# Kernel tuning notes

Hardware: AMD Instinct MI355X
Metric: run time of the kernel (lower is better)

Reference implementation:

```python
import jax, jax.numpy as jnp
import numpy as np

N_NODES = 100000
N_EDGES = 640000
H = 128

def setup_inputs() -> dict:
    key = jax.random.key(0)
    k = jax.random.split(key, 8)
    x_src = jax.random.normal(k[0], (N_NODES, H), dtype=jnp.float32)
    x_dst = jax.random.normal(k[1], (N_NODES, H), dtype=jnp.float32)
    src_idx = jax.random.randint(k[2], (N_EDGES,), 0, N_NODES, dtype=jnp.int64)
    dst_idx = jax.random.randint(k[3], (N_EDGES,), 0, N_NODES, dtype=jnp.int64)
    # torch Linear default init: U(-1/sqrt(fan_in), 1/sqrt(fan_in)); randn*scale is fine for a numeric baseline
    W1 = jax.random.normal(k[4], (H, 2 * H), dtype=jnp.float32) * (1.0 / np.sqrt(2 * H))
    b1 = jnp.zeros((H,), dtype=jnp.float32)
    W2 = jax.random.normal(k[5], (1, H), dtype=jnp.float32) * (1.0 / np.sqrt(H))
    b2 = jnp.zeros((1,), dtype=jnp.float32)
    return {"x_src": x_src, "x_dst": x_dst, "src_idx": src_idx, "dst_idx": dst_idx,
            "W1": W1, "b1": b1, "W2": W2, "b2": b2}

def reference(x_src, x_dst, src_idx, dst_idx, W1, b1, W2, b2):
    # per-edge gather of endpoint features, concat -> [E, 2H]
    h = jnp.concatenate([x_src[src_idx], x_dst[dst_idx]], axis=1)
    h = jax.nn.relu(h @ W1.T + b1)            # [E, H]
    score = (h @ W2.T + b2)[:, 0]             # [E]
    return score
```

## Files before the change

### kernel.cpp

```cpp
#include <hip/hip_runtime.h>
#include <hip/hip_bf16.h>

typedef __bf16 bf16x8 __attribute__((ext_vector_type(8)));
typedef float  f32x4  __attribute__((ext_vector_type(4)));

#define HF 128
#define W1K 256

__global__ __launch_bounds__(256, 2) void node_precompute_kernel(
    const float* __restrict__ x_src, const float* __restrict__ x_dst,
    const float* __restrict__ W1, const float* __restrict__ b1,
    __bf16* __restrict__ u, __bf16* __restrict__ v, int nNodes)
{
    __shared__ __align__(16) __bf16 wlds[32 * 64 * 8];

    const int which = blockIdx.y;
    const float* __restrict__ x = which ? x_dst : x_src;
    const float* __restrict__ W = W1 + (which ? HF : 0);
    __bf16* __restrict__ outp = which ? v : u;

    const int tid  = threadIdx.x;
    const int lane = tid & 63;
    const int wid  = tid >> 6;
    const int l15  = lane & 15;
    const int lg   = lane >> 4;

    for (int p = wid; p < 32; p += 4) {
        const int n  = p >> 2;
        const int kk = p & 3;
        const float* srcp = W + (n * 16 + l15) * W1K + kk * 32 + lg * 8;
        bf16x8 w8;
        #pragma unroll
        for (int i = 0; i < 8; ++i) w8[i] = (__bf16)srcp[i];
        *reinterpret_cast<bf16x8*>(&wlds[(p * 64 + lane) * 8]) = w8;
    }
    __syncthreads();

    const int rowbase = blockIdx.x * 256 + wid * 64;

    const float* rowp[4];
    #pragma unroll
    for (int m = 0; m < 4; ++m) {
        int row = rowbase + m * 16 + l15;
        row = min(row, nNodes - 1);
        rowp[m] = x + (size_t)row * HF + lg * 8;
    }

    f32x4 acc[4][8];
    #pragma unroll
    for (int m = 0; m < 4; ++m)
        #pragma unroll
        for (int n = 0; n < 8; ++n)
            acc[m][n] = (f32x4){0.f, 0.f, 0.f, 0.f};

    #pragma unroll
    for (int kk = 0; kk < 4; ++kk) {
        bf16x8 a[4];
        #pragma unroll
        for (int m = 0; m < 4; ++m) {
            const float* p = rowp[m] + kk * 32;
            f32x4 u0 = *reinterpret_cast<const f32x4*>(p);
            f32x4 u1 = *reinterpret_cast<const f32x4*>(p + 4);
            bf16x8 av;
            #pragma unroll
            for (int i = 0; i < 4; ++i) {
                av[i]     = (__bf16)u0[i];
                av[i + 4] = (__bf16)u1[i];
            }
            a[m] = av;
        }
        #pragma unroll
        for (int n = 0; n < 8; ++n) {
            bf16x8 bfrag = *reinterpret_cast<const bf16x8*>(
                &wlds[((n * 4 + kk) * 64 + lane) * 8]);
            #pragma unroll
            for (int m = 0; m < 4; ++m) {
                acc[m][n] = __builtin_amdgcn_mfma_f32_16x16x32_bf16(
                    a[m], bfrag, acc[m][n], 0, 0, 0);
            }
        }
    }

    float b1v[8];
    #pragma unroll
    for (int n = 0; n < 8; ++n)
        b1v[n] = (which == 0) ? b1[n * 16 + l15] : 0.f;

    #pragma unroll
    for (int m = 0; m < 4; ++m) {
        #pragma unroll
        for (int r = 0; r < 4; ++r) {
            const int row = rowbase + m * 16 + lg * 4 + r;
            if (row < nNodes) {
                #pragma unroll
                for (int n = 0; n < 8; ++n)
                    outp[(size_t)row * HF + n * 16 + l15] =
                        (__bf16)(acc[m][n][r] + b1v[n]);
            }
        }
    }
}

__global__ __launch_bounds__(256) void edge_score_kernel(
    const __bf16* __restrict__ u, const __bf16* __restrict__ v,
    const int* __restrict__ sidx, const int* __restrict__ didx,
    const float* __restrict__ W2, const float* __restrict__ b2,
    float* __restrict__ out, int nEdges)
{
    const int tid = threadIdx.x;
    const int sub = tid >> 4;
    const int l16 = tid & 15;

    const int e0 = blockIdx.x * 32 + sub;
    const int e1 = e0 + 16;
    const int c0 = min(e0, nEdges - 1);
    const int c1 = min(e1, nEdges - 1);

    float w2v[8];
    #pragma unroll
    for (int j = 0; j < 8; ++j) w2v[j] = W2[l16 * 8 + j];
    const float b2v = b2[0];

    const int si0 = sidx[c0], di0 = didx[c0];
    const int si1 = sidx[c1], di1 = didx[c1];

    const bf16x8 u0 = *reinterpret_cast<const bf16x8*>(u + (size_t)si0 * HF + l16 * 8);
    const bf16x8 v0 = *reinterpret_cast<const bf16x8*>(v + (size_t)di0 * HF + l16 * 8);
    const bf16x8 u1 = *reinterpret_cast<const bf16x8*>(u + (size_t)si1 * HF + l16 * 8);
    const bf16x8 v1 = *reinterpret_cast<const bf16x8*>(v + (size_t)di1 * HF + l16 * 8);

    float s0 = 0.f, s1 = 0.f;
    #pragma unroll
    for (int j = 0; j < 8; ++j) {
        s0 += fmaxf((float)u0[j] + (float)v0[j], 0.f) * w2v[j];
        s1 += fmaxf((float)u1[j] + (float)v1[j], 0.f) * w2v[j];
    }

    #pragma unroll
    for (int off = 1; off < 16; off <<= 1) {
        s0 += __shfl_xor(s0, off, 64);
        s1 += __shfl_xor(s1, off, 64);
    }

    if (l16 == 0) {
        if (e0 < nEdges) out[e0] = s0 + b2v;
        if (e1 < nEdges) out[e1] = s1 + b2v;
    }
}

__global__ __launch_bounds__(256, 2) void edge_mlp_kernel(
    const float* __restrict__ x_src, const float* __restrict__ x_dst,
    const int*   __restrict__ src_idx, const int* __restrict__ dst_idx,
    const float* __restrict__ W1, const float* __restrict__ b1,
    const float* __restrict__ W2, const float* __restrict__ b2,
    float* __restrict__ out, int nEdges)
{
    __shared__ __align__(16) __bf16 w1lds[64 * 64 * 8];

    const int tid  = threadIdx.x;
    const int lane = tid & 63;
    const int wid  = tid >> 6;
    const int l15  = lane & 15;
    const int lg   = lane >> 4;

    for (int p = wid; p < 64; p += 4) {
        const int n   = p >> 3;
        const int kk  = p & 7;
        const float* src = W1 + (n * 16 + l15) * W1K + kk * 32 + lg * 8;
        bf16x8 w8;
        #pragma unroll
        for (int i = 0; i < 8; ++i) w8[i] = (__bf16)src[i];
        *reinterpret_cast<bf16x8*>(&w1lds[(p * 64 + lane) * 8]) = w8;
    }
    __syncthreads();

    float w2v[8], b1v[8];
    #pragma unroll
    for (int n = 0; n < 8; ++n) {
        w2v[n] = W2[n * 16 + l15];
        b1v[n] = b1[n * 16 + l15];
    }
    const float b2v = b2[0];

    const int ntiles = nEdges / 256;
    for (int t = blockIdx.x; t < ntiles; t += gridDim.x) {
        const int ebase = t * 256 + wid * 64;

        const float* srow[4];
        const float* drow[4];
        #pragma unroll
        for (int m = 0; m < 4; ++m) {
            const int e  = ebase + m * 16 + l15;
            srow[m] = x_src + (size_t)src_idx[e] * HF + lg * 8;
            drow[m] = x_dst + (size_t)dst_idx[e] * HF + lg * 8;
        }

        f32x4 acc[4][8];
        #pragma unroll
        for (int m = 0; m < 4; ++m)
            #pragma unroll
            for (int n = 0; n < 8; ++n)
                acc[m][n] = (f32x4){0.f, 0.f, 0.f, 0.f};

        #pragma unroll
        for (int kk = 0; kk < 8; ++kk) {
            bf16x8 a[4];
            #pragma unroll
            for (int m = 0; m < 4; ++m) {
                const float* p = (kk < 4) ? (srow[m] + kk * 32)
                                          : (drow[m] + (kk - 4) * 32);
                f32x4 u0 = *reinterpret_cast<const f32x4*>(p);
                f32x4 u1 = *reinterpret_cast<const f32x4*>(p + 4);
                bf16x8 av;
                #pragma unroll
                for (int i = 0; i < 4; ++i) {
                    av[i]     = (__bf16)u0[i];
                    av[i + 4] = (__bf16)u1[i];
                }
                a[m] = av;
            }
            #pragma unroll
            for (int n = 0; n < 8; ++n) {
                bf16x8 bfrag = *reinterpret_cast<const bf16x8*>(
                    &w1lds[((n * 8 + kk) * 64 + lane) * 8]);
                #pragma unroll
                for (int m = 0; m < 4; ++m) {
                    acc[m][n] = __builtin_amdgcn_mfma_f32_16x16x32_bf16(
                        a[m], bfrag, acc[m][n], 0, 0, 0);
                }
            }
        }

        #pragma unroll
        for (int m = 0; m < 4; ++m) {
            float part[4];
            #pragma unroll
            for (int r = 0; r < 4; ++r) {
                float s = 0.f;
                #pragma unroll
                for (int n = 0; n < 8; ++n) {
                    float hv = acc[m][n][r] + b1v[n];
                    s += fmaxf(hv, 0.f) * w2v[n];
                }
                part[r] = s;
            }
            #pragma unroll
            for (int off = 1; off < 16; off <<= 1) {
                #pragma unroll
                for (int r = 0; r < 4; ++r)
                    part[r] += __shfl_xor(part[r], off, 64);
            }
            if (l15 == m) {
                f32x4 v4 = { part[0] + b2v, part[1] + b2v,
                             part[2] + b2v, part[3] + b2v };
                *reinterpret_cast<f32x4*>(&out[ebase + m * 16 + lg * 4]) = v4;
            }
        }
    }
}

extern "C" void kernel_launch(void* const* d_in, const int* in_sizes, int n_in,
                              void* d_out, int out_size, void* d_ws, size_t ws_size,
                              hipStream_t stream) {
    const float* x_src  = (const float*)d_in[0];
    const float* x_dst  = (const float*)d_in[1];
    const int*   sidx   = (const int*)d_in[2];
    const int*   didx   = (const int*)d_in[3];
    const float* W1     = (const float*)d_in[4];
    const float* b1     = (const float*)d_in[5];
    const float* W2     = (const float*)d_in[6];
    const float* b2     = (const float*)d_in[7];
    float* out = (float*)d_out;

    const int nEdges = in_sizes[2];
    const int nNodes = in_sizes[0] / HF;

    const size_t needed = (size_t)2 * nNodes * HF * sizeof(__bf16);
    if (ws_size >= needed) {
        __bf16* u = (__bf16*)d_ws;
        __bf16* v = u + (size_t)nNodes * HF;

        dim3 pgrid((nNodes + 255) / 256, 2);
        node_precompute_kernel<<<pgrid, 256, 0, stream>>>(
            x_src, x_dst, W1, b1, u, v, nNodes);

        const int egrid = (nEdges + 31) / 32;
        edge_score_kernel<<<egrid, 256, 0, stream>>>(
            u, v, sidx, didx, W2, b2, out, nEdges);
    } else {
        edge_mlp_kernel<<<512, 256, 0, stream>>>(
            x_src, x_dst, sidx, didx, W1, b1, W2, b2, out, nEdges);
    }
}
```

Measured before the change: 87.84 us.

## Transpose node-precompute MFMA for vectorized stores; batch four edges per edge thread

The node precompute kernel now treats W1 as the A operand and node features as B, so each lane holds four consecutive output features and writes them as one bf16x4 store instead of scattered scalar stores. Each wave now handles 16 nodes instead of 64, the grid grows to match, and launch bounds allow more resident blocks. The edge score kernel processes four edges per 16-lane group instead of two, giving more independent gathers in flight per thread. In exchange, each block reloads W1 into LDS for fewer nodes, and the edge kernel uses more registers per thread.

```diff
diff --git a/kernel.cpp b/kernel.cpp
--- a/kernel.cpp
+++ b/kernel.cpp
@@ -2,12 +2,13 @@
 #include <hip/hip_bf16.h>
 
 typedef __bf16 bf16x8 __attribute__((ext_vector_type(8)));
+typedef __bf16 bf16x4 __attribute__((ext_vector_type(4)));
 typedef float  f32x4  __attribute__((ext_vector_type(4)));
 
 #define HF 128
 #define W1K 256
 
-__global__ __launch_bounds__(256, 2) void node_precompute_kernel(
+__global__ __launch_bounds__(256, 4) void node_precompute2(
     const float* __restrict__ x_src, const float* __restrict__ x_dst,
     const float* __restrict__ W1, const float* __restrict__ b1,
     __bf16* __restrict__ u, __bf16* __restrict__ v, int nNodes)
@@ -26,9 +27,9 @@
     const int lg   = lane >> 4;
 
     for (int p = wid; p < 32; p += 4) {
-        const int n  = p >> 2;
+        const int mt = p >> 2;
         const int kk = p & 3;
-        const float* srcp = W + (n * 16 + l15) * W1K + kk * 32 + lg * 8;
+        const float* srcp = W + (mt * 16 + l15) * W1K + kk * 32 + lg * 8;
         bf16x8 w8;
         #pragma unroll
         for (int i = 0; i < 8; ++i) w8[i] = (__bf16)srcp[i];
@@ -36,67 +37,47 @@
     }
     __syncthreads();
 
-    const int rowbase = blockIdx.x * 256 + wid * 64;
-
-    const float* rowp[4];
-    #pragma unroll
-    for (int m = 0; m < 4; ++m) {
-        int row = rowbase + m * 16 + l15;
-        row = min(row, nNodes - 1);
-        rowp[m] = x + (size_t)row * HF + lg * 8;
-    }
-
-    f32x4 acc[4][8];
-    #pragma unroll
-    for (int m = 0; m < 4; ++m)
-        #pragma unroll
-        for (int n = 0; n < 8; ++n)
-            acc[m][n] = (f32x4){0.f, 0.f, 0.f, 0.f};
+    const int nbase = (blockIdx.x * 4 + wid) * 16;
+    int node = nbase + l15;
+    const int nodec = min(node, nNodes - 1);
+    const float* rowp = x + (size_t)nodec * HF + lg * 8;
+
+    f32x4 acc[8];
+    #pragma unroll
+    for (int mt = 0; mt < 8; ++mt) acc[mt] = (f32x4){0.f, 0.f, 0.f, 0.f};
 
     #pragma unroll
     for (int kk = 0; kk < 4; ++kk) {
-        bf16x8 a[4];
-        #pragma unroll
-        for (int m = 0; m < 4; ++m) {
-            const float* p = rowp[m] + kk * 32;
-            f32x4 u0 = *reinterpret_cast<const f32x4*>(p);
-            f32x4 u1 = *reinterpret_cast<const f32x4*>(p + 4);
-            bf16x8 av;
-            #pragma unroll
-            for (int i = 0; i < 4; ++i) {
-                av[i]     = (__bf16)u0[i];
-                av[i + 4] = (__bf16)u1[i];
-            }
-            a[m] = av;
-        }
-        #pragma unroll
-        for (int n = 0; n < 8; ++n) {
-            bf16x8 bfrag = *reinterpret_cast<const bf16x8*>(
-                &wlds[((n * 4 + kk) * 64 + lane) * 8]);
-            #pragma unroll
-            for (int m = 0; m < 4; ++m) {
-                acc[m][n] = __builtin_amdgcn_mfma_f32_16x16x32_bf16(
-                    a[m], bfrag, acc[m][n], 0, 0, 0);
-            }
-        }
-    }
-
-    float b1v[8];
-    #pragma unroll
-    for (int n = 0; n < 8; ++n)
-        b1v[n] = (which == 0) ? b1[n * 16 + l15] : 0.f;
-
-    #pragma unroll
-    for (int m = 0; m < 4; ++m) {
-        #pragma unroll
-        for (int r = 0; r < 4; ++r) {
-            const int row = rowbase + m * 16 + lg * 4 + r;
-            if (row < nNodes) {
-                #pragma unroll
-                for (int n = 0; n < 8; ++n)
-                    outp[(size_t)row * HF + n * 16 + l15] =
-                        (__bf16)(acc[m][n][r] + b1v[n]);
-            }
+        f32x4 u0 = *reinterpret_cast<const f32x4*>(rowp + kk * 32);
+        f32x4 u1 = *reinterpret_cast<const f32x4*>(rowp + kk * 32 + 4);
+        bf16x8 xb;
+        #pragma unroll
+        for (int i = 0; i < 4; ++i) {
+            xb[i]     = (__bf16)u0[i];
+            xb[i + 4] = (__bf16)u1[i];
+        }
+        #pragma unroll
+        for (int mt = 0; mt < 8; ++mt) {
+            bf16x8 wa = *reinterpret_cast<const bf16x8*>(
+                &wlds[((mt * 4 + kk) * 64 + lane) * 8]);
+            acc[mt] = __builtin_amdgcn_mfma_f32_16x16x32_bf16(
+                wa, xb, acc[mt], 0, 0, 0);
+        }
+    }
+
+    const int mynode = nbase + l15;
+    if (mynode < nNodes) {
+        __bf16* op = outp + (size_t)mynode * HF + lg * 4;
+        #pragma unroll
+        for (int mt = 0; mt < 8; ++mt) {
+            f32x4 b4 = {0.f, 0.f, 0.f, 0.f};
+            if (which == 0)
+                b4 = *reinterpret_cast<const f32x4*>(b1 + mt * 16 + lg * 4);
+            bf16x4 o4;
+            #pragma unroll
+            for (int r = 0; r < 4; ++r)
+                o4[r] = (__bf16)(acc[mt][r] + b4[r]);
+            *reinterpret_cast<bf16x4*>(op + mt * 16) = o4;
         }
     }
 }
@@ -111,40 +92,46 @@
     const int sub = tid >> 4;
     const int l16 = tid & 15;
 
-    const int e0 = blockIdx.x * 32 + sub;
-    const int e1 = e0 + 16;
-    const int c0 = min(e0, nEdges - 1);
-    const int c1 = min(e1, nEdges - 1);
+    const int ebase = blockIdx.x * 64 + sub;
 
     float w2v[8];
     #pragma unroll
     for (int j = 0; j < 8; ++j) w2v[j] = W2[l16 * 8 + j];
     const float b2v = b2[0];
 
-    const int si0 = sidx[c0], di0 = didx[c0];
-    const int si1 = sidx[c1], di1 = didx[c1];
-
-    const bf16x8 u0 = *reinterpret_cast<const bf16x8*>(u + (size_t)si0 * HF + l16 * 8);
-    const bf16x8 v0 = *reinterpret_cast<const bf16x8*>(v + (size_t)di0 * HF + l16 * 8);
-    const bf16x8 u1 = *reinterpret_cast<const bf16x8*>(u + (size_t)si1 * HF + l16 * 8);
-    const bf16x8 v1 = *reinterpret_cast<const bf16x8*>(v + (size_t)di1 * HF + l16 * 8);
-
-    float s0 = 0.f, s1 = 0.f;
-    #pragma unroll
-    for (int j = 0; j < 8; ++j) {
-        s0 += fmaxf((float)u0[j] + (float)v0[j], 0.f) * w2v[j];
-        s1 += fmaxf((float)u1[j] + (float)v1[j], 0.f) * w2v[j];
-    }
-
-    #pragma unroll
-    for (int off = 1; off < 16; off <<= 1) {
-        s0 += __shfl_xor(s0, off, 64);
-        s1 += __shfl_xor(s1, off, 64);
-    }
+    int e[4], si[4], di[4];
+    #pragma unroll
+    for (int q = 0; q < 4; ++q) {
+        e[q] = ebase + q * 16;
+        const int c = min(e[q], nEdges - 1);
+        si[q] = sidx[c];
+        di[q] = didx[c];
+    }
+
+    bf16x8 uv[4], vv[4];
+    #pragma unroll
+    for (int q = 0; q < 4; ++q) {
+        uv[q] = *reinterpret_cast<const bf16x8*>(u + (size_t)si[q] * HF + l16 * 8);
+        vv[q] = *reinterpret_cast<const bf16x8*>(v + (size_t)di[q] * HF + l16 * 8);
+    }
+
+    float s[4] = {0.f, 0.f, 0.f, 0.f};
+    #pragma unroll
+    for (int q = 0; q < 4; ++q)
+        #pragma unroll
+        for (int j = 0; j < 8; ++j)
+            s[q] += fmaxf((float)uv[q][j] + (float)vv[q][j], 0.f) * w2v[j];
+
+    #pragma unroll
+    for (int off = 1; off < 16; off <<= 1)
+        #pragma unroll
+        for (int q = 0; q < 4; ++q)
+            s[q] += __shfl_xor(s[q], off, 64);
 
     if (l16 == 0) {
-        if (e0 < nEdges) out[e0] = s0 + b2v;
-        if (e1 < nEdges) out[e1] = s1 + b2v;
+        #pragma unroll
+        for (int q = 0; q < 4; ++q)
+            if (e[q] < nEdges) out[e[q]] = s[q] + b2v;
     }
 }
 
@@ -280,11 +267,11 @@
         __bf16* u = (__bf16*)d_ws;
         __bf16* v = u + (size_t)nNodes * HF;
 
-        dim3 pgrid((nNodes + 255) / 256, 2);
-        node_precompute_kernel<<<pgrid, 256, 0, stream>>>(
+        dim3 pgrid((nNodes + 63) / 64, 2);
+        node_precompute2<<<pgrid, 256, 0, stream>>>(
             x_src, x_dst, W1, b1, u, v, nNodes);
 
-        const int egrid = (nEdges + 31) / 32;
+        const int egrid = (nEdges + 63) / 64;
         edge_score_kernel<<<egrid, 256, 0, stream>>>(
             u, v, sidx, didx, W2, b2, out, nEdges);
     } else {
```

Measured after the change: 105.3 us. +19.9%, slower.
